# Optimization experiments

Hardware: AMD Instinct MI355X
Metric: run time of the kernel (lower is better)

Reference implementation:

```python
import jax, jax.numpy as jnp
import numpy as np

D = 768        # word_emb_dim * 3 (span embedding dim)
H = 1024       # assumed FFNNScore hidden width
K = 250        # antecedent window (self.k)
P_LAMBDA = 0.4


def setup_inputs() -> dict:
    key = jax.random.key(0)
    ks = jax.random.split(key, 8)
    N, T = 2000, 1000
    return {
        "vectors": jax.random.normal(ks[0], (N, D), jnp.float32),
        "Wm1": jax.random.normal(ks[1], (D, H), jnp.float32) / np.sqrt(D),
        "bm1": jnp.zeros((H,), jnp.float32),
        "wm2": jax.random.normal(ks[2], (H,), jnp.float32) / np.sqrt(H),
        "bm2": jnp.zeros((1,), jnp.float32),
        "Wp1": jax.random.normal(ks[3], (3 * D, H), jnp.float32) / np.sqrt(3 * D),
        "bp1": jnp.zeros((H,), jnp.float32),
        "wp2": jax.random.normal(ks[4], (H,), jnp.float32) / np.sqrt(H),
        "bp2": jnp.zeros((1,), jnp.float32),
        "span_starts": jax.random.randint(ks[5], (N,), 0, T, dtype=jnp.int32),
        "span_ends": jax.random.randint(ks[6], (N,), 0, T, dtype=jnp.int32),
        "t": T,
    }


def reference(vectors, Wm1, bm1, wm2, bm2, Wp1, bp1, wp2, bp2,
              span_starts, span_ends, t):
    m = int(P_LAMBDA * t)  # number of retained spans (static)

    # mention scorer: FFNN over all span embeddings  [N]
    scores = jax.nn.relu(vectors @ Wm1 + bm1) @ wm2 + bm2[0]

    # prune to top int(p_lambda * t) spans by mention score (descending sort)
    top = jnp.argsort(-scores)[:m]
    s_top, v_top = scores[top], vectors[top]

    # re-sort retained spans by (i_start, i_end) descending
    order = jnp.lexsort((span_ends[top], span_starts[top]))[::-1]
    v, s = v_top[order], s_top[order]  # [m, D], [m]

    # pairwise scorer weight split for cat([a, b, a*b]) @ Wp1
    Wa, Wb, Wab = Wp1[:D], Wp1[D:2 * D], Wp1[2 * D:]

    # antecedent windows: span i vs spans i+1 .. i+K (padded/masked)
    idx = jnp.arange(m - 1)[:, None] + 1 + jnp.arange(K)[None, :]  # [m-1, K]
    valid = idx < m
    idxc = jnp.minimum(idx, m - 1)

    a = v[:m - 1]                      # [m-1, D]
    b = v[idxc]                        # [m-1, K, D]
    hb = (v @ Wb)[idxc]                # gather precomputed b-projection [m-1, K, H]
    h = jax.nn.relu((a @ Wa)[:, None, :] + hb
                    + jnp.einsum('ikd,dh->ikh', a[:, None, :] * b, Wab)
                    + bp1)             # [m-1, K, H]
    pairwise = h @ wp2 + bp2[0]        # [m-1, K]

    ant = pairwise + s[idxc] + s[:m - 1, None]
    ant = jnp.where(valid, ant, -jnp.inf)
    # dummy antecedent (epsilon) score 0 appended, then softmax per span
    full = jnp.concatenate([ant, jnp.zeros((m - 1, 1), ant.dtype)], axis=1)
    return jax.nn.softmax(full, axis=-1)  # [m-1, K+1]
```

## Files before the change

kernel.cpp:

```cpp
#include <hip/hip_runtime.h>
#include <hip/hip_bf16.h>
#include <math.h>

#define NVEC 2000
#define DD   768
#define HH   1024
#define KNUM 250
#define MSEL 400
#define MR   399
#define OUTW 251
#define PPAD 256
#define NPAIR (MR * PPAD)
#define BM 256
#define BN 256
#define BK 64
#define NKT (DD / BK)
#define NNB (HH / BN)

typedef short  bf16x8 __attribute__((ext_vector_type(8)));
typedef float  f32x4  __attribute__((ext_vector_type(4)));
typedef unsigned int u32;
typedef u32    u32x4  __attribute__((ext_vector_type(4)));

__device__ __forceinline__ float waveSum(float p) {
#pragma unroll
  for (int off = 32; off >= 1; off >>= 1) p += __shfl_xor(p, off, 64);
  return p;
}
__device__ __forceinline__ float waveMax(float p) {
#pragma unroll
  for (int off = 32; off >= 1; off >>= 1) p = fmaxf(p, __shfl_xor(p, off, 64));
  return p;
}
__device__ __forceinline__ short f2bf(float f) {
  __hip_bfloat16 h = __float2bfloat16(f);
  return __builtin_bit_cast(short, h);
}
__device__ __forceinline__ void gload_lds16(const void* g, void* l) {
  __builtin_amdgcn_global_load_lds(
      (const __attribute__((address_space(1))) u32*)g,
      (__attribute__((address_space(3))) u32*)l, 16, 0, 0);
}
__device__ __forceinline__ bf16x8 prodcvt(const float* av, bf16x8 b) {
  u32x4 u = __builtin_bit_cast(u32x4, b);
  bf16x8 r;
#pragma unroll
  for (int p = 0; p < 4; ++p) {
    const float blo = __builtin_bit_cast(float, u[p] << 16);
    const float bhi = __builtin_bit_cast(float, u[p] & 0xffff0000u);
    r[2 * p]     = f2bf(av[2 * p]     * blo);
    r[2 * p + 1] = f2bf(av[2 * p + 1] * bhi);
  }
  return r;
}

__global__ __launch_bounds__(512) void scores_kernel(
    const float* __restrict__ vectors, const float* __restrict__ Wm1,
    const float* __restrict__ bm1, const float* __restrict__ wm2,
    const float* __restrict__ bm2, float* __restrict__ scores) {
  __shared__ float vrow[4 * DD];
  __shared__ float red[8];
  const int tid = threadIdx.x;
  const int base = blockIdx.x * 4;
  for (int idx = tid; idx < 4 * DD; idx += 512)
    vrow[idx] = vectors[base * DD + idx];
  __syncthreads();
  float acc[4][2];
#pragma unroll
  for (int r = 0; r < 4; ++r) { acc[r][0] = 0.f; acc[r][1] = 0.f; }
#pragma unroll 2
  for (int d = 0; d < DD; d += 4) {
    float2 w0 = ((const float2*)(Wm1 + (size_t)(d + 0) * HH))[tid];
    float2 w1 = ((const float2*)(Wm1 + (size_t)(d + 1) * HH))[tid];
    float2 w2 = ((const float2*)(Wm1 + (size_t)(d + 2) * HH))[tid];
    float2 w3 = ((const float2*)(Wm1 + (size_t)(d + 3) * HH))[tid];
#pragma unroll
    for (int r = 0; r < 4; ++r) {
      const float4 a = *(const float4*)(vrow + r * DD + d);
      acc[r][0] += a.x * w0.x; acc[r][1] += a.x * w0.y;
      acc[r][0] += a.y * w1.x; acc[r][1] += a.y * w1.y;
      acc[r][0] += a.z * w2.x; acc[r][1] += a.z * w2.y;
      acc[r][0] += a.w * w3.x; acc[r][1] += a.w * w3.y;
    }
  }
  const float2 b = ((const float2*)bm1)[tid];
  const float2 m = ((const float2*)wm2)[tid];
  const float sc = bm2[0];
  for (int r = 0; r < 4; ++r) {
    float p = fmaxf(acc[r][0] + b.x, 0.f) * m.x + fmaxf(acc[r][1] + b.y, 0.f) * m.y;
    p = waveSum(p);
    if ((tid & 63) == 0) red[tid >> 6] = p;
    __syncthreads();
    if (tid == 0) {
      float t = red[0];
#pragma unroll
      for (int w8 = 1; w8 < 8; ++w8) t += red[w8];
      scores[base + r] = t + sc;
    }
    __syncthreads();
  }
}

__global__ __launch_bounds__(1024) void topsort_kernel(
    const float* __restrict__ scores, int* __restrict__ top) {
  __shared__ float ks[2048];
  __shared__ int   ki[2048];
  const int tid = threadIdx.x;
  for (int e = tid; e < 2048; e += 1024) {
    ks[e] = (e < NVEC) ? scores[e] : -INFINITY;
    ki[e] = e;
  }
  __syncthreads();
  for (int k = 2; k <= 2048; k <<= 1) {
    for (int j = k >> 1; j > 0; j >>= 1) {
      for (int e = tid; e < 2048; e += 1024) {
        const int l = e ^ j;
        if (l > e) {
          const float s1 = ks[e], s2 = ks[l];
          const int i1 = ki[e], i2 = ki[l];
          const bool first = (s1 > s2) || (s1 == s2 && i1 < i2);
          const bool up = ((e & k) == 0);
          if (up ? !first : first) {
            ks[e] = s2; ks[l] = s1; ki[e] = i2; ki[l] = i1;
          }
        }
      }
      __syncthreads();
    }
  }
  if (tid < MSEL) top[tid] = ki[tid];
}

__global__ __launch_bounds__(256) void lexsort_kernel(
    const int* __restrict__ top, const int* __restrict__ sst,
    const int* __restrict__ sen, const float* __restrict__ scores,
    int* __restrict__ perm, float* __restrict__ sfin) {
  __shared__ int s_st[512], s_en[512], s_j[512];
  const int tid = threadIdx.x;
  for (int e = tid; e < 512; e += 256) {
    if (e < MSEL) { const int ti = top[e]; s_st[e] = sst[ti]; s_en[e] = sen[ti]; }
    else { s_st[e] = 0x7fffffff; s_en[e] = 0x7fffffff; }
    s_j[e] = e;
  }
  __syncthreads();
  for (int k = 2; k <= 512; k <<= 1) {
    for (int j = k >> 1; j > 0; j >>= 1) {
      for (int e = tid; e < 512; e += 256) {
        const int l = e ^ j;
        if (l > e) {
          const int a0 = s_st[e], a1 = s_en[e], a2 = s_j[e];
          const int b0 = s_st[l], b1 = s_en[l], b2 = s_j[l];
          const bool first = (a0 < b0) || (a0 == b0 && (a1 < b1 || (a1 == b1 && a2 < b2)));
          const bool up = ((e & k) == 0);
          if (up ? !first : first) {
            s_st[e] = b0; s_en[e] = b1; s_j[e] = b2;
            s_st[l] = a0; s_en[l] = a1; s_j[l] = a2;
          }
        }
      }
      __syncthreads();
    }
  }
  for (int i = tid; i < MSEL; i += 256) {
    const int src = s_j[MSEL - 1 - i];
    const int vi = top[src];
    perm[i] = vi;
    sfin[i] = scores[vi];
  }
}

__global__ __launch_bounds__(256) void hab_kernel(
    const float* __restrict__ vectors, const float* __restrict__ Wp1,
    const int* __restrict__ perm, float* __restrict__ Ha, float* __restrict__ Hv,
    float* __restrict__ Vp, ushort* __restrict__ Vpb) {
  __shared__ float vrow[4 * DD];
  const int tid = threadIdx.x;
  const int base = blockIdx.x * 4;
  const int mat = blockIdx.y >> 1;
  const int half = blockIdx.y & 1;
  for (int r = 0; r < 4; ++r) {
    const int pi = perm[base + r];
    for (int d = tid; d < DD; d += 256) {
      const float val = vectors[pi * DD + d];
      vrow[r * DD + d] = val;
      if (blockIdx.y == 0) {
        Vp[(size_t)(base + r) * DD + d] = val;
        Vpb[(size_t)(base + r) * DD + d] = (ushort)f2bf(val);
      }
    }
  }
  __syncthreads();
  float acc[4][2];
#pragma unroll
  for (int r = 0; r < 4; ++r) { acc[r][0] = 0.f; acc[r][1] = 0.f; }
  const float* W = Wp1 + (size_t)mat * DD * HH + half * 512;
#pragma unroll 2
  for (int d = 0; d < DD; d += 4) {
    float2 w0 = ((const float2*)(W + (size_t)(d + 0) * HH))[tid];
    float2 w1 = ((const float2*)(W + (size_t)(d + 1) * HH))[tid];
    float2 w2 = ((const float2*)(W + (size_t)(d + 2) * HH))[tid];
    float2 w3 = ((const float2*)(W + (size_t)(d + 3) * HH))[tid];
#pragma unroll
    for (int r = 0; r < 4; ++r) {
      const float4 a = *(const float4*)(vrow + r * DD + d);
      acc[r][0] += a.x * w0.x; acc[r][1] += a.x * w0.y;
      acc[r][0] += a.y * w1.x; acc[r][1] += a.y * w1.y;
      acc[r][0] += a.z * w2.x; acc[r][1] += a.z * w2.y;
      acc[r][0] += a.w * w3.x; acc[r][1] += a.w * w3.y;
    }
  }
  float* dst = mat ? Hv : Ha;
  for (int r = 0; r < 4; ++r) {
    const int row = base + r;
    if (mat == 0 && row >= MR) continue;
    ((float2*)(dst + (size_t)row * HH + half * 512))[tid] =
        make_float2(acc[r][0], acc[r][1]);
  }
}

__global__ __launch_bounds__(256) void wt_kernel(
    const float* __restrict__ Wp1, ushort* __restrict__ Wt) {
  __shared__ float tile[64][65];
  const int kb = blockIdx.x;
  const int nb = blockIdx.y;
  const float* Wab = Wp1 + 2 * DD * HH;
  for (int idx = threadIdx.x; idx < 64 * 64; idx += 256) {
    const int kk = idx >> 6, nn = idx & 63;
    tile[kk][nn] = Wab[(size_t)(kb * 64 + kk) * HH + nb * 64 + nn];
  }
  __syncthreads();
  for (int idx = threadIdx.x; idx < 64 * 64; idx += 256) {
    const int nn = idx >> 6, kk = idx & 63;
    Wt[(size_t)(nb * 64 + nn) * DD + kb * 64 + kk] = (ushort)f2bf(tile[kk][nn]);
  }
}

__global__ __launch_bounds__(512, 2) void pair_kernel(
    const float* __restrict__ Vp, const ushort* __restrict__ Vpb,
    const ushort* __restrict__ Wt,
    const float* __restrict__ bp1, const float* __restrict__ wp2,
    const float* __restrict__ Ha, const float* __restrict__ Hv,
    float* __restrict__ pp) {
  __shared__ __align__(16) ushort As[2][BM * BK];
  __shared__ __align__(16) ushort Bs[2][BN * BK];
  __shared__ float redp[BM][4];
  const int tid = threadIdx.x;
  const int i = blockIdx.x;
  const int nb = blockIdx.y;
  const int n0 = nb * BN;
  const int lane = tid & 63;
  const int wid = tid >> 6;
  const int wr = wid >> 2, wc = wid & 3;
  const int lhi = lane >> 4, llo = lane & 15;

  const int cs = tid & 7;
  const int rbase = tid >> 3;
  const int csx = cs ^ (rbase & 7);
  const ushort* vsrc[4];
  int rowA[4];
#pragma unroll
  for (int it = 0; it < 4; ++it) {
    rowA[it] = it * 64 + rbase;
    int j = i + 1 + rowA[it];
    if (j > MR) j = MR;
    vsrc[it] = Vpb + (size_t)j * DD + cs * 8;
  }
  const float* avp = Vp + (size_t)i * DD + cs * 8;

  f32x4 acc[8][4];
#pragma unroll
  for (int a = 0; a < 8; ++a)
#pragma unroll
    for (int b = 0; b < 4; ++b) acc[a][b] = (f32x4){0.f, 0.f, 0.f, 0.f};

#pragma unroll
  for (int it = 0; it < 4; ++it) {
    gload_lds16(Wt + (size_t)(n0 + rowA[it]) * DD + csx * 8,
                (char*)Bs[0] + (it * 512 + tid) * 16);
  }
  {
    float av[8];
    *(float4*)(av) = *(const float4*)(avp);
    *(float4*)(av + 4) = *(const float4*)(avp + 4);
#pragma unroll
    for (int it = 0; it < 4; ++it) {
      const bf16x8 bv = *(const bf16x8*)(vsrc[it]);
      *(bf16x8*)((char*)As[0] + rowA[it] * 128 + (csx << 4)) = prodcvt(av, bv);
    }
  }
  __syncthreads();

  int cur = 0;
  for (int kt = 0; kt < NKT; ++kt) {
    const bool has_next = (kt + 1 < NKT);
    const int kgn = (kt + 1) * BK;
    bf16x8 bvn[4];
    float avn[8];
    if (has_next) {
      char* Bn = (char*)Bs[cur ^ 1];
#pragma unroll
      for (int it = 0; it < 4; ++it) {
        gload_lds16(Wt + (size_t)(n0 + rowA[it]) * DD + kgn + csx * 8,
                    Bn + (it * 512 + tid) * 16);
      }
#pragma unroll
      for (int it = 0; it < 4; ++it) bvn[it] = *(const bf16x8*)(vsrc[it] + kgn);
      *(float4*)(avn) = *(const float4*)(avp + kgn);
      *(float4*)(avn + 4) = *(const float4*)(avp + kgn + 4);
    }
    const char* Ab = (const char*)As[cur];
    const char* Bb = (const char*)Bs[cur];
#pragma unroll
    for (int ks = 0; ks < 2; ++ks) {
      bf16x8 af[8], bfr[4];
#pragma unroll
      for (int mi = 0; mi < 8; ++mi) {
        const int row = wr * 128 + mi * 16 + llo;
        const int ch = (ks * 4 + lhi) ^ (row & 7);
        af[mi] = *(const bf16x8*)(Ab + row * 128 + (ch << 4));
      }
#pragma unroll
      for (int ni = 0; ni < 4; ++ni) {
        const int row = wc * 64 + ni * 16 + llo;
        const int ch = (ks * 4 + lhi) ^ (row & 7);
        bfr[ni] = *(const bf16x8*)(Bb + row * 128 + (ch << 4));
      }
#pragma unroll
      for (int mi = 0; mi < 8; ++mi)
#pragma unroll
        for (int ni = 0; ni < 4; ++ni)
          acc[mi][ni] = __builtin_amdgcn_mfma_f32_16x16x32_bf16(af[mi], bfr[ni], acc[mi][ni], 0, 0, 0);
    }
    if (has_next) {
      char* An = (char*)As[cur ^ 1];
#pragma unroll
      for (int it = 0; it < 4; ++it)
        *(bf16x8*)(An + rowA[it] * 128 + (csx << 4)) = prodcvt(avn, bvn[it]);
    }
    __syncthreads();
    cur ^= 1;
  }

  float hb4[4], wpv[4];
  int cg[4];
#pragma unroll
  for (int ni = 0; ni < 4; ++ni) {
    const int col = n0 + wc * 64 + ni * 16 + llo;
    cg[ni] = col;
    hb4[ni] = Ha[(size_t)i * HH + col] + bp1[col];
    wpv[ni] = wp2[col];
  }
#pragma unroll
  for (int mi = 0; mi < 8; ++mi) {
#pragma unroll
    for (int r = 0; r < 4; ++r) {
      const int rowl = wr * 128 + mi * 16 + lhi * 4 + r;
      int j = i + 1 + rowl;
      if (j > MR) j = MR;
      float part = 0.f;
#pragma unroll
      for (int ni = 0; ni < 4; ++ni) {
        const float pre = acc[mi][ni][r] + hb4[ni] + Hv[(size_t)j * HH + cg[ni]];
        part += fmaxf(pre, 0.f) * wpv[ni];
      }
      part += __shfl_xor(part, 1, 64);
      part += __shfl_xor(part, 2, 64);
      part += __shfl_xor(part, 4, 64);
      part += __shfl_xor(part, 8, 64);
      if (llo == 0) redp[rowl][wc] = part;
    }
  }
  __syncthreads();
  if (tid < BM)
    pp[(size_t)nb * NPAIR + (size_t)i * PPAD + tid] =
        redp[tid][0] + redp[tid][1] + redp[tid][2] + redp[tid][3];
}

__global__ __launch_bounds__(256) void softmax_kernel(
    const float* __restrict__ pp, const float* __restrict__ sfin,
    const float* __restrict__ bp2, float* __restrict__ out) {
  __shared__ float red[4];
  const int i = blockIdx.x, tid = threadIdx.x;
  float v;
  if (tid < KNUM) {
    const int jidx = i + 1 + tid;
    const bool valid = jidx < MSEL;
    const int jc = valid ? jidx : MR;
    float s = 0.f;
#pragma unroll
    for (int b = 0; b < NNB; ++b) s += pp[(size_t)b * NPAIR + i * PPAD + tid];
    v = valid ? (s + bp2[0] + sfin[jc] + sfin[i]) : -INFINITY;
  } else if (tid == KNUM) v = 0.f;
  else v = -INFINITY;
  float mx = waveMax(v);
  if ((tid & 63) == 0) red[tid >> 6] = mx;
  __syncthreads();
  const float m = fmaxf(fmaxf(red[0], red[1]), fmaxf(red[2], red[3]));
  __syncthreads();
  const float e = (tid <= KNUM) ? expf(v - m) : 0.f;
  float s = waveSum(e);
  if ((tid & 63) == 0) red[tid >> 6] = s;
  __syncthreads();
  const float tot = red[0] + red[1] + red[2] + red[3];
  if (tid <= KNUM) out[i * OUTW + tid] = e / tot;
}

extern "C" void kernel_launch(void* const* d_in, const int* in_sizes, int n_in,
                              void* d_out, int out_size, void* d_ws, size_t ws_size,
                              hipStream_t stream) {
  const float* vectors = (const float*)d_in[0];
  const float* Wm1 = (const float*)d_in[1];
  const float* bm1 = (const float*)d_in[2];
  const float* wm2 = (const float*)d_in[3];
  const float* bm2 = (const float*)d_in[4];
  const float* Wp1 = (const float*)d_in[5];
  const float* bp1 = (const float*)d_in[6];
  const float* wp2 = (const float*)d_in[7];
  const float* bp2 = (const float*)d_in[8];
  const int* sst = (const int*)d_in[9];
  const int* sen = (const int*)d_in[10];
  float* out = (float*)d_out;
  char* ws = (char*)d_ws;

  float* scores = (float*)(ws);
  int*   top    = (int*)(ws + 8192);
  int*   perm   = (int*)(ws + 10240);
  float* sfin   = (float*)(ws + 12288);
  float* Ha     = (float*)(ws + 16384);
  float* Hv     = (float*)(ws + 16384 + 1638400);
  float* Vp     = (float*)(ws + 3293184);
  ushort* Wt    = (ushort*)(ws + 4521984);
  ushort* Vpb   = (ushort*)(ws + 6094848);
  float* pp     = (float*)(ws + 6709248);

  scores_kernel<<<NVEC / 4, 512, 0, stream>>>(vectors, Wm1, bm1, wm2, bm2, scores);
  topsort_kernel<<<1, 1024, 0, stream>>>(scores, top);
  lexsort_kernel<<<1, 256, 0, stream>>>(top, sst, sen, scores, perm, sfin);
  wt_kernel<<<dim3(12, 16), 256, 0, stream>>>(Wp1, Wt);
  hab_kernel<<<dim3(MSEL / 4, 4), 256, 0, stream>>>(vectors, Wp1, perm, Ha, Hv, Vp, Vpb);
  pair_kernel<<<dim3(MR, NNB), 512, 0, stream>>>(Vp, Vpb, Wt, bp1, wp2, Ha, Hv, pp);
  softmax_kernel<<<MR, 256, 0, stream>>>(pp, sfin, bp2, out);
}
```

Measured before the change: 441.0 us.

## Triple-buffer weight tiles with fine-grained waitcnt and single A buffer in pair GEMM

The pair kernel now streams the Wab weight tiles through a three-stage LDS ring, prefetching two K-steps ahead with direct-to-LDS loads, and keeps a single A buffer that is rewritten after a barrier. Each full __syncthreads is replaced by explicit s_waitcnt vmcnt/lgkmcnt plus s_barrier, so only the older loads are waited on. MFMA sections also get raised wave priority via s_setprio. The aim is to hide global-load latency for B behind compute. The cost is an extra barrier per iteration to protect the single A buffer, and the hand-counted vmcnt values must match the outstanding loads exactly or the results will be wrong.

```diff
diff --git a/kernel.cpp b/kernel.cpp
--- a/kernel.cpp
+++ b/kernel.cpp
@@ -241,8 +241,8 @@
     const float* __restrict__ bp1, const float* __restrict__ wp2,
     const float* __restrict__ Ha, const float* __restrict__ Hv,
     float* __restrict__ pp) {
-  __shared__ __align__(16) ushort As[2][BM * BK];
-  __shared__ __align__(16) ushort Bs[2][BN * BK];
+  __shared__ __align__(16) ushort As[BM * BK];
+  __shared__ __align__(16) ushort Bs[3][BN * BK];
   __shared__ float redp[BM][4];
   const int tid = threadIdx.x;
   const int i = blockIdx.x;
@@ -273,43 +273,52 @@
 #pragma unroll
     for (int b = 0; b < 4; ++b) acc[a][b] = (f32x4){0.f, 0.f, 0.f, 0.f};
 
-#pragma unroll
-  for (int it = 0; it < 4; ++it) {
-    gload_lds16(Wt + (size_t)(n0 + rowA[it]) * DD + csx * 8,
-                (char*)Bs[0] + (it * 512 + tid) * 16);
-  }
   {
     float av[8];
+    bf16x8 bv[4];
     *(float4*)(av) = *(const float4*)(avp);
     *(float4*)(av + 4) = *(const float4*)(avp + 4);
 #pragma unroll
-    for (int it = 0; it < 4; ++it) {
-      const bf16x8 bv = *(const bf16x8*)(vsrc[it]);
-      *(bf16x8*)((char*)As[0] + rowA[it] * 128 + (csx << 4)) = prodcvt(av, bv);
-    }
-  }
-  __syncthreads();
-
-  int cur = 0;
+    for (int it = 0; it < 4; ++it) bv[it] = *(const bf16x8*)(vsrc[it]);
+    __builtin_amdgcn_sched_barrier(0);
+#pragma unroll
+    for (int it = 0; it < 4; ++it)
+      gload_lds16(Wt + (size_t)(n0 + rowA[it]) * DD + csx * 8,
+                  (char*)Bs[0] + (it * 512 + tid) * 16);
+#pragma unroll
+    for (int it = 0; it < 4; ++it)
+      gload_lds16(Wt + (size_t)(n0 + rowA[it]) * DD + BK + csx * 8,
+                  (char*)Bs[1] + (it * 512 + tid) * 16);
+#pragma unroll
+    for (int it = 0; it < 4; ++it)
+      *(bf16x8*)((char*)As + rowA[it] * 128 + (csx << 4)) = prodcvt(av, bv[it]);
+    asm volatile("s_waitcnt vmcnt(4) lgkmcnt(0)" ::: "memory");
+    __builtin_amdgcn_s_barrier();
+  }
+
   for (int kt = 0; kt < NKT; ++kt) {
-    const bool has_next = (kt + 1 < NKT);
-    const int kgn = (kt + 1) * BK;
+    const int cb = kt % 3;
     bf16x8 bvn[4];
     float avn[8];
-    if (has_next) {
-      char* Bn = (char*)Bs[cur ^ 1];
-#pragma unroll
-      for (int it = 0; it < 4; ++it) {
-        gload_lds16(Wt + (size_t)(n0 + rowA[it]) * DD + kgn + csx * 8,
-                    Bn + (it * 512 + tid) * 16);
-      }
+    const int kgn = (kt + 1) * BK;
+    if (kt + 1 < NKT) {
 #pragma unroll
       for (int it = 0; it < 4; ++it) bvn[it] = *(const bf16x8*)(vsrc[it] + kgn);
       *(float4*)(avn) = *(const float4*)(avp + kgn);
       *(float4*)(avn + 4) = *(const float4*)(avp + kgn + 4);
     }
-    const char* Ab = (const char*)As[cur];
-    const char* Bb = (const char*)Bs[cur];
+    __builtin_amdgcn_sched_barrier(0);
+    if (kt + 2 < NKT) {
+      const int kgn2 = (kt + 2) * BK;
+      char* Bn = (char*)Bs[(kt + 2) % 3];
+#pragma unroll
+      for (int it = 0; it < 4; ++it)
+        gload_lds16(Wt + (size_t)(n0 + rowA[it]) * DD + kgn2 + csx * 8,
+                    Bn + (it * 512 + tid) * 16);
+    }
+    const char* Ab = (const char*)As;
+    const char* Bb = (const char*)Bs[cb];
+    __builtin_amdgcn_s_setprio(1);
 #pragma unroll
     for (int ks = 0; ks < 2; ++ks) {
       bf16x8 af[8], bfr[4];
@@ -331,14 +340,20 @@
         for (int ni = 0; ni < 4; ++ni)
           acc[mi][ni] = __builtin_amdgcn_mfma_f32_16x16x32_bf16(af[mi], bfr[ni], acc[mi][ni], 0, 0, 0);
     }
-    if (has_next) {
-      char* An = (char*)As[cur ^ 1];
+    __builtin_amdgcn_s_setprio(0);
+    asm volatile("s_waitcnt lgkmcnt(0)" ::: "memory");
+    __builtin_amdgcn_s_barrier();
+    if (kt + 1 < NKT) {
 #pragma unroll
       for (int it = 0; it < 4; ++it)
-        *(bf16x8*)(An + rowA[it] * 128 + (csx << 4)) = prodcvt(avn, bvn[it]);
-    }
-    __syncthreads();
-    cur ^= 1;
+        *(bf16x8*)((char*)As + rowA[it] * 128 + (csx << 4)) = prodcvt(avn, bvn[it]);
+    }
+    if (kt < NKT - 2) {
+      asm volatile("s_waitcnt vmcnt(4) lgkmcnt(0)" ::: "memory");
+    } else {
+      asm volatile("s_waitcnt vmcnt(0) lgkmcnt(0)" ::: "memory");
+    }
+    __builtin_amdgcn_s_barrier();
   }
 
   float hb4[4], wpv[4];
```

After: 460.2 us. +4.4%, slower.

## Single-buffer pair GEMM LDS for higher occupancy; widen row blocking in score kernels

Applied to the files above, without the earlier changes.

The pair kernel drops LDS double buffering and asks for 4 blocks per CU instead of 2, so more waves can overlap global loads with MFMA work through occupancy instead of software prefetch. The scores and hab kernels now process 8 rows per block instead of 4, halving the number of times each weight is reloaded, and their inner loop reads one weight row per step. The risks are register spills under the tighter launch bound, exposed load latency now that prefetch is gone, and fewer blocks in the smaller kernels.

```diff
diff --git a/kernel.cpp b/kernel.cpp
--- a/kernel.cpp
+++ b/kernel.cpp
@@ -58,35 +58,29 @@
     const float* __restrict__ vectors, const float* __restrict__ Wm1,
     const float* __restrict__ bm1, const float* __restrict__ wm2,
     const float* __restrict__ bm2, float* __restrict__ scores) {
-  __shared__ float vrow[4 * DD];
+  __shared__ float vrow[8 * DD];
   __shared__ float red[8];
   const int tid = threadIdx.x;
-  const int base = blockIdx.x * 4;
-  for (int idx = tid; idx < 4 * DD; idx += 512)
+  const int base = blockIdx.x * 8;
+  for (int idx = tid; idx < 8 * DD; idx += 512)
     vrow[idx] = vectors[base * DD + idx];
   __syncthreads();
-  float acc[4][2];
-#pragma unroll
-  for (int r = 0; r < 4; ++r) { acc[r][0] = 0.f; acc[r][1] = 0.f; }
-#pragma unroll 2
-  for (int d = 0; d < DD; d += 4) {
-    float2 w0 = ((const float2*)(Wm1 + (size_t)(d + 0) * HH))[tid];
-    float2 w1 = ((const float2*)(Wm1 + (size_t)(d + 1) * HH))[tid];
-    float2 w2 = ((const float2*)(Wm1 + (size_t)(d + 2) * HH))[tid];
-    float2 w3 = ((const float2*)(Wm1 + (size_t)(d + 3) * HH))[tid];
-#pragma unroll
-    for (int r = 0; r < 4; ++r) {
-      const float4 a = *(const float4*)(vrow + r * DD + d);
-      acc[r][0] += a.x * w0.x; acc[r][1] += a.x * w0.y;
-      acc[r][0] += a.y * w1.x; acc[r][1] += a.y * w1.y;
-      acc[r][0] += a.z * w2.x; acc[r][1] += a.z * w2.y;
-      acc[r][0] += a.w * w3.x; acc[r][1] += a.w * w3.y;
+  float acc[8][2];
+#pragma unroll
+  for (int r = 0; r < 8; ++r) { acc[r][0] = 0.f; acc[r][1] = 0.f; }
+#pragma unroll 4
+  for (int d = 0; d < DD; ++d) {
+    const float2 w = ((const float2*)(Wm1 + (size_t)d * HH))[tid];
+#pragma unroll
+    for (int r = 0; r < 8; ++r) {
+      const float a = vrow[r * DD + d];
+      acc[r][0] += a * w.x; acc[r][1] += a * w.y;
     }
   }
   const float2 b = ((const float2*)bm1)[tid];
   const float2 m = ((const float2*)wm2)[tid];
   const float sc = bm2[0];
-  for (int r = 0; r < 4; ++r) {
+  for (int r = 0; r < 8; ++r) {
     float p = fmaxf(acc[r][0] + b.x, 0.f) * m.x + fmaxf(acc[r][1] + b.y, 0.f) * m.y;
     p = waveSum(p);
     if ((tid & 63) == 0) red[tid >> 6] = p;
@@ -173,12 +167,12 @@
     const float* __restrict__ vectors, const float* __restrict__ Wp1,
     const int* __restrict__ perm, float* __restrict__ Ha, float* __restrict__ Hv,
     float* __restrict__ Vp, ushort* __restrict__ Vpb) {
-  __shared__ float vrow[4 * DD];
+  __shared__ float vrow[8 * DD];
   const int tid = threadIdx.x;
-  const int base = blockIdx.x * 4;
+  const int base = blockIdx.x * 8;
   const int mat = blockIdx.y >> 1;
   const int half = blockIdx.y & 1;
-  for (int r = 0; r < 4; ++r) {
+  for (int r = 0; r < 8; ++r) {
     const int pi = perm[base + r];
     for (int d = tid; d < DD; d += 256) {
       const float val = vectors[pi * DD + d];
@@ -190,27 +184,21 @@
     }
   }
   __syncthreads();
-  float acc[4][2];
-#pragma unroll
-  for (int r = 0; r < 4; ++r) { acc[r][0] = 0.f; acc[r][1] = 0.f; }
+  float acc[8][2];
+#pragma unroll
+  for (int r = 0; r < 8; ++r) { acc[r][0] = 0.f; acc[r][1] = 0.f; }
   const float* W = Wp1 + (size_t)mat * DD * HH + half * 512;
-#pragma unroll 2
-  for (int d = 0; d < DD; d += 4) {
-    float2 w0 = ((const float2*)(W + (size_t)(d + 0) * HH))[tid];
-    float2 w1 = ((const float2*)(W + (size_t)(d + 1) * HH))[tid];
-    float2 w2 = ((const float2*)(W + (size_t)(d + 2) * HH))[tid];
-    float2 w3 = ((const float2*)(W + (size_t)(d + 3) * HH))[tid];
-#pragma unroll
-    for (int r = 0; r < 4; ++r) {
-      const float4 a = *(const float4*)(vrow + r * DD + d);
-      acc[r][0] += a.x * w0.x; acc[r][1] += a.x * w0.y;
-      acc[r][0] += a.y * w1.x; acc[r][1] += a.y * w1.y;
-      acc[r][0] += a.z * w2.x; acc[r][1] += a.z * w2.y;
-      acc[r][0] += a.w * w3.x; acc[r][1] += a.w * w3.y;
+#pragma unroll 4
+  for (int d = 0; d < DD; ++d) {
+    const float2 w = ((const float2*)(W + (size_t)d * HH))[tid];
+#pragma unroll
+    for (int r = 0; r < 8; ++r) {
+      const float a = vrow[r * DD + d];
+      acc[r][0] += a * w.x; acc[r][1] += a * w.y;
     }
   }
   float* dst = mat ? Hv : Ha;
-  for (int r = 0; r < 4; ++r) {
+  for (int r = 0; r < 8; ++r) {
     const int row = base + r;
     if (mat == 0 && row >= MR) continue;
     ((float2*)(dst + (size_t)row * HH + half * 512))[tid] =
@@ -235,14 +223,14 @@
   }
 }
 
-__global__ __launch_bounds__(512, 2) void pair_kernel(
+__global__ __launch_bounds__(512, 4) void pair_kernel(
     const float* __restrict__ Vp, const ushort* __restrict__ Vpb,
     const ushort* __restrict__ Wt,
     const float* __restrict__ bp1, const float* __restrict__ wp2,
     const float* __restrict__ Ha, const float* __restrict__ Hv,
     float* __restrict__ pp) {
-  __shared__ __align__(16) ushort As[2][BM * BK];
-  __shared__ __align__(16) ushort Bs[2][BN * BK];
+  __shared__ __align__(16) ushort As[BM * BK];
+  __shared__ __align__(16) ushort Bs[BN * BK];
   __shared__ float redp[BM][4];
   const int tid = threadIdx.x;
   const int i = blockIdx.x;
@@ -273,43 +261,22 @@
 #pragma unroll
     for (int b = 0; b < 4; ++b) acc[a][b] = (f32x4){0.f, 0.f, 0.f, 0.f};
 
-#pragma unroll
-  for (int it = 0; it < 4; ++it) {
-    gload_lds16(Wt + (size_t)(n0 + rowA[it]) * DD + csx * 8,
-                (char*)Bs[0] + (it * 512 + tid) * 16);
-  }
-  {
+  for (int kt = 0; kt < NKT; ++kt) {
+    const int kg = kt * BK;
+    bf16x8 bv[4];
     float av[8];
-    *(float4*)(av) = *(const float4*)(avp);
-    *(float4*)(av + 4) = *(const float4*)(avp + 4);
-#pragma unroll
-    for (int it = 0; it < 4; ++it) {
-      const bf16x8 bv = *(const bf16x8*)(vsrc[it]);
-      *(bf16x8*)((char*)As[0] + rowA[it] * 128 + (csx << 4)) = prodcvt(av, bv);
-    }
-  }
-  __syncthreads();
-
-  int cur = 0;
-  for (int kt = 0; kt < NKT; ++kt) {
-    const bool has_next = (kt + 1 < NKT);
-    const int kgn = (kt + 1) * BK;
-    bf16x8 bvn[4];
-    float avn[8];
-    if (has_next) {
-      char* Bn = (char*)Bs[cur ^ 1];
-#pragma unroll
-      for (int it = 0; it < 4; ++it) {
-        gload_lds16(Wt + (size_t)(n0 + rowA[it]) * DD + kgn + csx * 8,
-                    Bn + (it * 512 + tid) * 16);
-      }
-#pragma unroll
-      for (int it = 0; it < 4; ++it) bvn[it] = *(const bf16x8*)(vsrc[it] + kgn);
-      *(float4*)(avn) = *(const float4*)(avp + kgn);
-      *(float4*)(avn + 4) = *(const float4*)(avp + kgn + 4);
-    }
-    const char* Ab = (const char*)As[cur];
-    const char* Bb = (const char*)Bs[cur];
+#pragma unroll
+    for (int it = 0; it < 4; ++it) bv[it] = *(const bf16x8*)(vsrc[it] + kg);
+    *(float4*)(av) = *(const float4*)(avp + kg);
+    *(float4*)(av + 4) = *(const float4*)(avp + kg + 4);
+#pragma unroll
+    for (int it = 0; it < 4; ++it)
+      gload_lds16(Wt + (size_t)(n0 + rowA[it]) * DD + kg + csx * 8,
+                  (char*)Bs + (it * 512 + tid) * 16);
+#pragma unroll
+    for (int it = 0; it < 4; ++it)
+      *(bf16x8*)((char*)As + rowA[it] * 128 + (csx << 4)) = prodcvt(av, bv[it]);
+    __syncthreads();
 #pragma unroll
     for (int ks = 0; ks < 2; ++ks) {
       bf16x8 af[8], bfr[4];
@@ -317,13 +284,13 @@
       for (int mi = 0; mi < 8; ++mi) {
         const int row = wr * 128 + mi * 16 + llo;
         const int ch = (ks * 4 + lhi) ^ (row & 7);
-        af[mi] = *(const bf16x8*)(Ab + row * 128 + (ch << 4));
+        af[mi] = *(const bf16x8*)((const char*)As + row * 128 + (ch << 4));
       }
 #pragma unroll
       for (int ni = 0; ni < 4; ++ni) {
         const int row = wc * 64 + ni * 16 + llo;
         const int ch = (ks * 4 + lhi) ^ (row & 7);
-        bfr[ni] = *(const bf16x8*)(Bb + row * 128 + (ch << 4));
+        bfr[ni] = *(const bf16x8*)((const char*)Bs + row * 128 + (ch << 4));
       }
 #pragma unroll
       for (int mi = 0; mi < 8; ++mi)
@@ -331,14 +298,7 @@
         for (int ni = 0; ni < 4; ++ni)
           acc[mi][ni] = __builtin_amdgcn_mfma_f32_16x16x32_bf16(af[mi], bfr[ni], acc[mi][ni], 0, 0, 0);
     }
-    if (has_next) {
-      char* An = (char*)As[cur ^ 1];
-#pragma unroll
-      for (int it = 0; it < 4; ++it)
-        *(bf16x8*)(An + rowA[it] * 128 + (csx << 4)) = prodcvt(avn, bvn[it]);
-    }
     __syncthreads();
-    cur ^= 1;
   }
 
   float hb4[4], wpv[4];
@@ -433,11 +393,11 @@
   ushort* Vpb   = (ushort*)(ws + 6094848);
   float* pp     = (float*)(ws + 6709248);
 
-  scores_kernel<<<NVEC / 4, 512, 0, stream>>>(vectors, Wm1, bm1, wm2, bm2, scores);
+  scores_kernel<<<NVEC / 8, 512, 0, stream>>>(vectors, Wm1, bm1, wm2, bm2, scores);
   topsort_kernel<<<1, 1024, 0, stream>>>(scores, top);
   lexsort_kernel<<<1, 256, 0, stream>>>(top, sst, sen, scores, perm, sfin);
   wt_kernel<<<dim3(12, 16), 256, 0, stream>>>(Wp1, Wt);
-  hab_kernel<<<dim3(MSEL / 4, 4), 256, 0, stream>>>(vectors, Wp1, perm, Ha, Hv, Vp, Vpb);
+  hab_kernel<<<dim3(MSEL / 8, 4), 256, 0, stream>>>(vectors, Wp1, perm, Ha, Hv, Vp, Vpb);
   pair_kernel<<<dim3(MR, NNB), 512, 0, stream>>>(Vp, Vpb, Wt, bp1, wp2, Ha, Hv, pp);
   softmax_kernel<<<MR, 256, 0, stream>>>(pp, sfin, bp2, out);
 }
```

After: 1.281 ms. 2.91x slower.
